# Performance work log

Measured on AMD Instinct MI355X. Metric: run time of the kernel, lower is better.

## Reference

```python
import jax, jax.numpy as jnp
import numpy as np

EPS = 1e-12  # torch F.normalize default eps


def setup_inputs() -> dict:
    key = jax.random.key(0)
    k1, k2, k3, k4 = jax.random.split(key, 4)
    dim, heads, b, h, w = 192, 6, 2, 48, 48
    scale = 1.0 / np.sqrt(dim)
    return {
        "inp": jax.random.normal(k1, (b, dim, h, w), dtype=jnp.float32),
        "wq": jax.random.normal(k2, (dim, dim), dtype=jnp.float32) * scale,
        "wk": jax.random.normal(k3, (dim, dim), dtype=jnp.float32) * scale,
        "wv": jax.random.normal(k4, (dim, dim), dtype=jnp.float32) * scale,
        "temperature": jnp.ones((heads, 1, 1), dtype=jnp.float32),
    }


def _l2norm_lastdim(x):
    # torch F.normalize(x, dim=-1): x / max(||x||_2, eps)
    n = jnp.sqrt(jnp.sum(x * x, axis=-1, keepdims=True))
    return x / jnp.maximum(n, EPS)


def reference(inp, wq, wk, wv, temperature):
    b, c, h, w = inp.shape
    heads = temperature.shape[0]
    ch = c // heads
    n = h * w
    x = inp.reshape(b, c, n)  # 1x1 conv == channel matmul
    q = jnp.einsum("oc,bcn->bon", wq, x).reshape(b, heads, ch, n)
    k = jnp.einsum("oc,bcn->bon", wk, x).reshape(b, heads, ch, n)
    v = jnp.einsum("oc,bcn->bon", wv, x).reshape(b, heads, ch, n)
    q = _l2norm_lastdim(q)
    k = _l2norm_lastdim(k)
    # k^T @ q over channel dim -> [b, heads, n, n]; temperature [heads,1,1] broadcasts
    attn = jnp.einsum("bhcn,bhcm->bhnm", k, q) * temperature
    attn = jax.nn.softmax(attn, axis=-1)
    return attn, v
```

## Files before the change

### kernel.cpp

```cpp
#include <hip/hip_runtime.h>
#include <hip/hip_bf16.h>
#include <cstdint>

#define NSP   2304
#define NT    144
#define ATTN_ELEMS 63700992

typedef __attribute__((ext_vector_type(8))) __bf16 bf16x8;
typedef __attribute__((ext_vector_type(4))) float  float4v;

__device__ __forceinline__ unsigned short f2bf(float f) {
  union { float f; unsigned int u; } v; v.f = f;
  unsigned int u = v.u;
  unsigned int r = u + 0x7FFFu + ((u >> 16) & 1u);
  return (unsigned short)(r >> 16);
}

__device__ __forceinline__ float bf2f(unsigned int bits16) {
  union { unsigned int u; float f; } v; v.u = bits16 << 16; return v.f;
}

__global__ __launch_bounds__(256) void prep_pack(
    const float* __restrict__ wq, const float* __restrict__ wk,
    const float* __restrict__ wv, const float* __restrict__ x,
    unsigned short* __restrict__ Wp, unsigned short* __restrict__ Xp,
    float* __restrict__ sums)
{
  int t = blockIdx.x * 256 + threadIdx.x;
  if (t < 768) sums[t] = 0.f;
  int lane = t & 63;
  int g = t >> 6;
  int quad = lane >> 4, col = lane & 15;
  union { int4 v; unsigned short u[8]; } o;
  if (g < 216) {
    int mt = g / 6, kc = g % 6;
    int oo = mt * 16 + col;
    int c0 = kc * 32 + quad * 8;
    const float* w = (oo < 192) ? (wq + (size_t)oo * 192)
                   : (oo < 384) ? (wk + (size_t)(oo - 192) * 192)
                                : (wv + (size_t)(oo - 384) * 192);
#pragma unroll
    for (int jj = 0; jj < 8; ++jj) o.u[jj] = f2bf(w[c0 + jj]);
    ((int4*)Wp)[(size_t)g * 64 + lane] = o.v;
  } else {
    int gx = g - 216;
    int kc = gx % 6;
    int bnt = gx / 6;
    int b = bnt / 144;
    int n = (bnt % 144) * 16 + col;
    int c0 = kc * 32 + quad * 8;
    const float* xp = x + ((size_t)b * 192 + c0) * NSP + n;
#pragma unroll
    for (int jj = 0; jj < 8; ++jj) o.u[jj] = f2bf(xp[(size_t)jj * NSP]);
    ((int4*)Xp)[(size_t)gx * 64 + lane] = o.v;
  }
}

__global__ __launch_bounds__(256) void proj_mfma(
    const bf16x8* __restrict__ Wp, const bf16x8* __restrict__ Xp,
    float* __restrict__ qws, float* __restrict__ kws, float* __restrict__ vout,
    float* __restrict__ sums)
{
  int lane = threadIdx.x & 63, w = threadIdx.x >> 6;
  int ng = blockIdx.x * 4 + w;
  int mt = blockIdx.y;
  int b  = blockIdx.z;
  int nt0 = ng * 4;
  float4v acc0 = {0.f,0.f,0.f,0.f};
  float4v acc1 = acc0, acc2 = acc0, acc3 = acc0;
#pragma unroll
  for (int kc = 0; kc < 6; ++kc) {
    bf16x8 a = Wp[(size_t)(mt * 6 + kc) * 64 + lane];
    const bf16x8* xb = Xp + (size_t)((b * 144 + nt0) * 6 + kc) * 64 + lane;
    acc0 = __builtin_amdgcn_mfma_f32_16x16x32_bf16(a, xb[0],    acc0, 0, 0, 0);
    acc1 = __builtin_amdgcn_mfma_f32_16x16x32_bf16(a, xb[384],  acc1, 0, 0, 0);
    acc2 = __builtin_amdgcn_mfma_f32_16x16x32_bf16(a, xb[768],  acc2, 0, 0, 0);
    acc3 = __builtin_amdgcn_mfma_f32_16x16x32_bf16(a, xb[1152], acc3, 0, 0, 0);
  }
  int quad = lane >> 4, col = lane & 15;
  int o0 = mt * 16 + quad * 4;
  float* dst;
  if (mt < 12)      dst = qws + ((size_t)b * 192 + o0) * NSP;
  else if (mt < 24) dst = kws + ((size_t)b * 192 + (o0 - 192)) * NSP;
  else              dst = vout + ((size_t)b * 192 + (o0 - 384)) * NSP;
  float4v acc[4] = {acc0, acc1, acc2, acc3};
#pragma unroll
  for (int tt = 0; tt < 4; ++tt)
#pragma unroll
    for (int r = 0; r < 4; ++r)
      dst[(size_t)r * NSP + (nt0 + tt) * 16 + col] = acc[tt][r];

  if (mt < 24) {
    int rbase = (mt < 12) ? (b * 192 + o0) : (384 + b * 192 + (o0 - 192));
#pragma unroll
    for (int r = 0; r < 4; ++r) {
      float p = acc0[r]*acc0[r] + acc1[r]*acc1[r]
              + acc2[r]*acc2[r] + acc3[r]*acc3[r];
#pragma unroll
      for (int off = 1; off < 16; off <<= 1) p += __shfl_xor(p, off);
      if (col == 0) atomicAdd(&sums[rbase + r], p);
    }
  }
}

__global__ __launch_bounds__(256) void packqk(
    const float* __restrict__ qws, const float* __restrict__ kws,
    const float* __restrict__ sums,
    unsigned short* __restrict__ Qp, unsigned short* __restrict__ Kp)
{
  int which = blockIdx.z;
  int bh = blockIdx.y;
  int nc = blockIdx.x;
  const float* src = which ? kws : qws;
  int b = bh / 6, h = bh % 6;
  __shared__ float xs[32][65];
  __shared__ float ivs[32];
  int t = threadIdx.x;
  if (t < 32) {
    float sm = sums[which * 384 + b * 192 + h * 32 + t];
    ivs[t] = 1.0f / fmaxf(sqrtf(sm), 1e-12f);
  }
  __syncthreads();
  const float* base = src + ((size_t)b * 192 + h * 32) * NSP + nc * 64;
#pragma unroll
  for (int i = 0; i < 8; ++i) {
    int idx = t + 256 * i;
    int ch = idx >> 6, nl = idx & 63;
    xs[ch][nl] = base[(size_t)ch * NSP + nl] * ivs[ch];
  }
  __syncthreads();
  int jl = t >> 6, lane = t & 63, quad = lane >> 4, col = lane & 15;
  int jt = nc * 4 + jl;
  union { int4 v; unsigned short u[8]; } o;
#pragma unroll
  for (int jj = 0; jj < 8; ++jj) o.u[jj] = f2bf(xs[quad * 8 + jj][jl * 16 + col]);
  int4* dst = (int4*)(which ? Kp : Qp);
  dst[(size_t)(bh * 144 + jt) * 64 + lane] = o.v;
}

__global__ __launch_bounds__(512) void attn_kernel(
    const bf16x8* __restrict__ Qp, const bf16x8* __restrict__ Kp,
    const float* __restrict__ temp, float* __restrict__ out)
{
  int lane = threadIdx.x & 63, w = threadIdx.x >> 6;
  int itile = blockIdx.x;
  int bh = blockIdx.y;
  float T = temp[bh % 6];
  bf16x8 kf = Kp[((size_t)bh * NT + itile) * 64 + lane];
  const bf16x8* qb = Qp + (size_t)bh * NT * 64 + lane;

  unsigned int ec[36];
  float s = 0.f;
#pragma unroll
  for (int u = 0; u < 18; ++u) {
    int jt = w + 8 * u;
    bf16x8 qf = qb[(size_t)jt * 64];
    float4v acc = {0.f,0.f,0.f,0.f};
    acc = __builtin_amdgcn_mfma_f32_16x16x32_bf16(qf, kf, acc, 0, 0, 0);
    float e0 = __expf(acc[0] * T);
    float e1 = __expf(acc[1] * T);
    float e2 = __expf(acc[2] * T);
    float e3 = __expf(acc[3] * T);
    s += (e0 + e1) + (e2 + e3);
    ec[2*u]   = (unsigned int)f2bf(e0) | ((unsigned int)f2bf(e1) << 16);
    ec[2*u+1] = (unsigned int)f2bf(e2) | ((unsigned int)f2bf(e3) << 16);
  }
  s += __shfl_xor(s, 16);
  s += __shfl_xor(s, 32);
  __shared__ float ls[8][16];
  if (lane < 16) ls[w][lane] = s;
  __syncthreads();
  int col = lane & 15, quad = lane >> 4;
  float tot = 0.f;
#pragma unroll
  for (int ww = 0; ww < 8; ++ww) tot += ls[ww][col];
  float inv = 1.0f / tot;

  __shared__ float xs[16][260];
  float* obase = out + (size_t)bh * NSP * NSP + (size_t)(itile * 16) * NSP;
  for (int c = 0; c < 9; ++c) {
#pragma unroll
    for (int ul = 0; ul < 2; ++ul) {
      int u = 2 * c + ul;
      unsigned int p0 = ec[2*u], p1 = ec[2*u+1];
      float4v o4;
      o4[0] = bf2f(p0 & 0xffffu) * inv;
      o4[1] = bf2f(p0 >> 16)     * inv;
      o4[2] = bf2f(p1 & 0xffffu) * inv;
      o4[3] = bf2f(p1 >> 16)     * inv;
      *(float4v*)&xs[col][(ul * 8 + w) * 16 + quad * 4] = o4;
    }
    __syncthreads();
#pragma unroll
    for (int rr = 0; rr < 2; ++rr) {
      int row = w + rr * 8;
      float4v o4 = *(const float4v*)&xs[row][lane * 4];
      *(float4v*)(obase + (size_t)row * NSP + c * 256 + lane * 4) = o4;
    }
    __syncthreads();
  }
}

extern "C" void kernel_launch(void* const* d_in, const int* in_sizes, int n_in,
                              void* d_out, int out_size, void* d_ws, size_t ws_size,
                              hipStream_t stream) {
  const float* x    = (const float*)d_in[0];
  const float* wq   = (const float*)d_in[1];
  const float* wk   = (const float*)d_in[2];
  const float* wv   = (const float*)d_in[3];
  const float* temp = (const float*)d_in[4];

  float* attn_out = (float*)d_out;
  float* vout     = attn_out + (size_t)ATTN_ELEMS;

  float* qws = (float*)d_ws;
  float* kws = qws + 884736;
  float* sums = kws + 884736;
  unsigned short* Wp = (unsigned short*)(sums + 768);
  unsigned short* Xp = Wp + 110592;
  unsigned short* Qp = Xp + 884736;
  unsigned short* Kp = Qp + 884736;

  hipLaunchKernelGGL(prep_pack, dim3(486), dim3(256), 0, stream,
                     wq, wk, wv, x, Wp, Xp, sums);
  hipLaunchKernelGGL(proj_mfma, dim3(9, 36, 2), dim3(256), 0, stream,
                     (const bf16x8*)Wp, (const bf16x8*)Xp, qws, kws, vout, sums);
  hipLaunchKernelGGL(packqk, dim3(36, 12, 2), dim3(256), 0, stream,
                     qws, kws, sums, Qp, Kp);
  hipLaunchKernelGGL(attn_kernel, dim3(144, 12), dim3(512), 0, stream,
                     (const bf16x8*)Qp, (const bf16x8*)Kp, temp, attn_out);
}
```

Baseline: 279.7 us.

## Fuse Q/K bf16 packing into projection and defer normalization to attention

The projection kernel now computes two 16-row output tiles per block, so each block covers a full head's 32 channels. It transposes Q/K results through shared memory and writes bf16 fragments directly, which removes the packqk kernel and the fp32 Q/K workspace round-trip. Because the L2 norms are not known inside the projection, Q and K are packed unnormalized. The attention kernel folds the combined inverse norms of q and k into the K fragment before the MFMA. This drops one launch and about 14 MB of intermediate traffic, at the cost of an extra bf16 rounding on K and possible precision loss from packing unnormalized values.

```diff
diff --git a/kernel.cpp b/kernel.cpp
--- a/kernel.cpp
+++ b/kernel.cpp
@@ -58,95 +58,109 @@
 
 __global__ __launch_bounds__(256) void proj_mfma(
     const bf16x8* __restrict__ Wp, const bf16x8* __restrict__ Xp,
-    float* __restrict__ qws, float* __restrict__ kws, float* __restrict__ vout,
-    float* __restrict__ sums)
+    unsigned short* __restrict__ Qp, unsigned short* __restrict__ Kp,
+    float* __restrict__ vout, float* __restrict__ sums)
 {
   int lane = threadIdx.x & 63, w = threadIdx.x >> 6;
-  int ng = blockIdx.x * 4 + w;
-  int mt = blockIdx.y;
-  int b  = blockIdx.z;
-  int nt0 = ng * 4;
-  float4v acc0 = {0.f,0.f,0.f,0.f};
-  float4v acc1 = acc0, acc2 = acc0, acc3 = acc0;
+  int xblk = blockIdx.x;
+  int y    = blockIdx.y;
+  int b    = blockIdx.z;
+  int nt0  = xblk * 16 + w * 4;
+  int mt0  = y * 2;
+  float4v acc[2][4];
+#pragma unroll
+  for (int t = 0; t < 2; ++t)
+#pragma unroll
+    for (int tt = 0; tt < 4; ++tt) acc[t][tt] = float4v{0.f,0.f,0.f,0.f};
 #pragma unroll
   for (int kc = 0; kc < 6; ++kc) {
-    bf16x8 a = Wp[(size_t)(mt * 6 + kc) * 64 + lane];
+    bf16x8 a0 = Wp[(size_t)(mt0 * 6 + kc) * 64 + lane];
+    bf16x8 a1 = Wp[(size_t)((mt0 + 1) * 6 + kc) * 64 + lane];
     const bf16x8* xb = Xp + (size_t)((b * 144 + nt0) * 6 + kc) * 64 + lane;
-    acc0 = __builtin_amdgcn_mfma_f32_16x16x32_bf16(a, xb[0],    acc0, 0, 0, 0);
-    acc1 = __builtin_amdgcn_mfma_f32_16x16x32_bf16(a, xb[384],  acc1, 0, 0, 0);
-    acc2 = __builtin_amdgcn_mfma_f32_16x16x32_bf16(a, xb[768],  acc2, 0, 0, 0);
-    acc3 = __builtin_amdgcn_mfma_f32_16x16x32_bf16(a, xb[1152], acc3, 0, 0, 0);
+#pragma unroll
+    for (int tt = 0; tt < 4; ++tt) {
+      bf16x8 bfr = xb[(size_t)tt * 384];
+      acc[0][tt] = __builtin_amdgcn_mfma_f32_16x16x32_bf16(a0, bfr, acc[0][tt], 0, 0, 0);
+      acc[1][tt] = __builtin_amdgcn_mfma_f32_16x16x32_bf16(a1, bfr, acc[1][tt], 0, 0, 0);
+    }
   }
   int quad = lane >> 4, col = lane & 15;
-  int o0 = mt * 16 + quad * 4;
-  float* dst;
-  if (mt < 12)      dst = qws + ((size_t)b * 192 + o0) * NSP;
-  else if (mt < 24) dst = kws + ((size_t)b * 192 + (o0 - 192)) * NSP;
-  else              dst = vout + ((size_t)b * 192 + (o0 - 384)) * NSP;
-  float4v acc[4] = {acc0, acc1, acc2, acc3};
-#pragma unroll
-  for (int tt = 0; tt < 4; ++tt)
-#pragma unroll
-    for (int r = 0; r < 4; ++r)
-      dst[(size_t)r * NSP + (nt0 + tt) * 16 + col] = acc[tt][r];
-
-  if (mt < 24) {
-    int rbase = (mt < 12) ? (b * 192 + o0) : (384 + b * 192 + (o0 - 192));
+
+  if (y >= 12) {
+    float* dst = vout + ((size_t)b * 192 + (y - 12) * 32) * NSP;
+#pragma unroll
+    for (int t = 0; t < 2; ++t)
+#pragma unroll
+      for (int tt = 0; tt < 4; ++tt)
+#pragma unroll
+        for (int r = 0; r < 4; ++r)
+          dst[(size_t)(t * 16 + quad * 4 + r) * NSP + (nt0 + tt) * 16 + col] = acc[t][tt][r];
+    return;
+  }
+
+  int isK = (y >= 6) ? 1 : 0;
+  int h = isK ? (y - 6) : y;
+  int sbase = isK * 384 + b * 192 + h * 32;
+#pragma unroll
+  for (int t = 0; t < 2; ++t)
 #pragma unroll
     for (int r = 0; r < 4; ++r) {
-      float p = acc0[r]*acc0[r] + acc1[r]*acc1[r]
-              + acc2[r]*acc2[r] + acc3[r]*acc3[r];
+      float p = acc[t][0][r] * acc[t][0][r] + acc[t][1][r] * acc[t][1][r]
+              + acc[t][2][r] * acc[t][2][r] + acc[t][3][r] * acc[t][3][r];
 #pragma unroll
       for (int off = 1; off < 16; off <<= 1) p += __shfl_xor(p, off);
-      if (col == 0) atomicAdd(&sums[rbase + r], p);
-    }
-  }
-}
-
-__global__ __launch_bounds__(256) void packqk(
-    const float* __restrict__ qws, const float* __restrict__ kws,
-    const float* __restrict__ sums,
-    unsigned short* __restrict__ Qp, unsigned short* __restrict__ Kp)
-{
-  int which = blockIdx.z;
-  int bh = blockIdx.y;
-  int nc = blockIdx.x;
-  const float* src = which ? kws : qws;
-  int b = bh / 6, h = bh % 6;
-  __shared__ float xs[32][65];
-  __shared__ float ivs[32];
-  int t = threadIdx.x;
-  if (t < 32) {
-    float sm = sums[which * 384 + b * 192 + h * 32 + t];
-    ivs[t] = 1.0f / fmaxf(sqrtf(sm), 1e-12f);
-  }
+      if (col == 0) atomicAdd(&sums[sbase + t * 16 + quad * 4 + r], p);
+    }
+
+  __shared__ float xs[32][257];
+#pragma unroll
+  for (int t = 0; t < 2; ++t)
+#pragma unroll
+    for (int tt = 0; tt < 4; ++tt)
+#pragma unroll
+      for (int r = 0; r < 4; ++r)
+        xs[t * 16 + quad * 4 + r][(w * 4 + tt) * 16 + col] = acc[t][tt][r];
   __syncthreads();
-  const float* base = src + ((size_t)b * 192 + h * 32) * NSP + nc * 64;
-#pragma unroll
-  for (int i = 0; i < 8; ++i) {
-    int idx = t + 256 * i;
-    int ch = idx >> 6, nl = idx & 63;
-    xs[ch][nl] = base[(size_t)ch * NSP + nl] * ivs[ch];
-  }
-  __syncthreads();
-  int jl = t >> 6, lane = t & 63, quad = lane >> 4, col = lane & 15;
-  int jt = nc * 4 + jl;
-  union { int4 v; unsigned short u[8]; } o;
-#pragma unroll
-  for (int jj = 0; jj < 8; ++jj) o.u[jj] = f2bf(xs[quad * 8 + jj][jl * 16 + col]);
-  int4* dst = (int4*)(which ? Kp : Qp);
-  dst[(size_t)(bh * 144 + jt) * 64 + lane] = o.v;
+
+  unsigned short* Pp = isK ? Kp : Qp;
+  int bh = b * 6 + h;
+#pragma unroll
+  for (int i = 0; i < 4; ++i) {
+    int jtl = w + 4 * i;
+    union { int4 v; unsigned short u[8]; } o;
+#pragma unroll
+    for (int jj = 0; jj < 8; ++jj) o.u[jj] = f2bf(xs[quad * 8 + jj][jtl * 16 + col]);
+    ((int4*)Pp)[(size_t)(bh * 144 + xblk * 16 + jtl) * 64 + lane] = o.v;
+  }
 }
 
 __global__ __launch_bounds__(512) void attn_kernel(
     const bf16x8* __restrict__ Qp, const bf16x8* __restrict__ Kp,
-    const float* __restrict__ temp, float* __restrict__ out)
+    const float* __restrict__ sums, const float* __restrict__ temp,
+    float* __restrict__ out)
 {
   int lane = threadIdx.x & 63, w = threadIdx.x >> 6;
   int itile = blockIdx.x;
   int bh = blockIdx.y;
+  int quad = lane >> 4, col = lane & 15;
   float T = temp[bh % 6];
-  bf16x8 kf = Kp[((size_t)bh * NT + itile) * 64 + lane];
+
+  __shared__ float gs[32];
+  if (threadIdx.x < 32) {
+    int bq = bh / 6, hq = bh % 6;
+    float sq = sums[bq * 192 + hq * 32 + threadIdx.x];
+    float sk = sums[384 + bq * 192 + hq * 32 + threadIdx.x];
+    gs[threadIdx.x] = (1.0f / fmaxf(sqrtf(sq), 1e-12f))
+                    * (1.0f / fmaxf(sqrtf(sk), 1e-12f));
+  }
+  __syncthreads();
+
+  union { bf16x8 v; unsigned short u[8]; } kr, ks;
+  kr.v = Kp[((size_t)bh * NT + itile) * 64 + lane];
+#pragma unroll
+  for (int jj = 0; jj < 8; ++jj)
+    ks.u[jj] = f2bf(bf2f(kr.u[jj]) * gs[quad * 8 + jj]);
+  bf16x8 kf = ks.v;
   const bf16x8* qb = Qp + (size_t)bh * NT * 64 + lane;
 
   unsigned int ec[36];
@@ -170,7 +184,6 @@
   __shared__ float ls[8][16];
   if (lane < 16) ls[w][lane] = s;
   __syncthreads();
-  int col = lane & 15, quad = lane >> 4;
   float tot = 0.f;
 #pragma unroll
   for (int ww = 0; ww < 8; ++ww) tot += ls[ww][col];
@@ -213,9 +226,7 @@
   float* attn_out = (float*)d_out;
   float* vout     = attn_out + (size_t)ATTN_ELEMS;
 
-  float* qws = (float*)d_ws;
-  float* kws = qws + 884736;
-  float* sums = kws + 884736;
+  float* sums = (float*)d_ws;
   unsigned short* Wp = (unsigned short*)(sums + 768);
   unsigned short* Xp = Wp + 110592;
   unsigned short* Qp = Xp + 884736;
@@ -223,10 +234,8 @@
 
   hipLaunchKernelGGL(prep_pack, dim3(486), dim3(256), 0, stream,
                      wq, wk, wv, x, Wp, Xp, sums);
-  hipLaunchKernelGGL(proj_mfma, dim3(9, 36, 2), dim3(256), 0, stream,
-                     (const bf16x8*)Wp, (const bf16x8*)Xp, qws, kws, vout, sums);
-  hipLaunchKernelGGL(packqk, dim3(36, 12, 2), dim3(256), 0, stream,
-                     qws, kws, sums, Qp, Kp);
+  hipLaunchKernelGGL(proj_mfma, dim3(9, 18, 2), dim3(256), 0, stream,
+                     (const bf16x8*)Wp, (const bf16x8*)Xp, Qp, Kp, vout, sums);
   hipLaunchKernelGGL(attn_kernel, dim3(144, 12), dim3(512), 0, stream,
-                     (const bf16x8*)Qp, (const bf16x8*)Kp, temp, attn_out);
-}
+                     (const bf16x8*)Qp, (const bf16x8*)Kp, sums, temp, attn_out);
+}
```

Measured after the change: 274.9 us. No clear change (-1.7%).
